# Kernel tuning notes

Hardware: AMD Instinct MI355X
Metric: run time of the kernel (lower is better)

## Reference

```python
import jax, jax.numpy as jnp
import numpy as np

WINDOW_SIZE = 11
SIGMA = 1.5


def _make_window(channel):
    # 1D gaussian, normalized, then outer product -> (C, 1, K, K) depthwise kernel
    xs = np.arange(WINDOW_SIZE) - WINDOW_SIZE // 2
    g = np.exp(-(xs ** 2) / (2.0 * SIGMA ** 2))
    g = g / g.sum()
    w2d = np.outer(g, g).astype(np.float32)
    w = np.broadcast_to(w2d[None, None], (channel, 1, WINDOW_SIZE, WINDOW_SIZE))
    return jnp.asarray(np.ascontiguousarray(w))


def _dwconv(x, window, channel):
    # depthwise valid conv, NCHW layout, groups = channel
    return jax.lax.conv_general_dilated(
        x, window,
        window_strides=(1, 1), padding='VALID',
        dimension_numbers=('NCHW', 'OIHW', 'NCHW'),
        feature_group_count=channel)


def setup_inputs() -> dict:
    key = jax.random.key(0)
    k1, k2 = jax.random.split(key)
    img1 = jax.random.uniform(k1, (32, 3, 512, 512), dtype=jnp.float32)
    img2 = jax.random.uniform(k2, (32, 3, 512, 512), dtype=jnp.float32)
    return {"img1": img1, "img2": img2}


def reference(img1, img2):
    channel = img1.shape[1]
    window = _make_window(channel).astype(img1.dtype)

    # dynamic range heuristic (val_range is None in the module's usage)
    max_val = jnp.where(jnp.max(img1) > 128, 255.0, 1.0)
    min_val = jnp.where(jnp.min(img1) < -0.5, -1.0, 0.0)
    L = max_val - min_val

    mu1 = _dwconv(img1, window, channel)
    mu2 = _dwconv(img2, window, channel)
    mu1_sq = mu1 * mu1
    mu2_sq = mu2 * mu2
    mu1_mu2 = mu1 * mu2

    sigma1_sq = _dwconv(img1 * img1, window, channel) - mu1_sq
    sigma2_sq = _dwconv(img2 * img2, window, channel) - mu2_sq
    sigma12 = _dwconv(img1 * img2, window, channel) - mu1_mu2

    C1 = (0.01 * L) ** 2
    C2 = (0.03 * L) ** 2
    ssim_map = ((2 * mu1_mu2 + C1) * (2 * sigma12 + C2)) / (
        (mu1_sq + mu2_sq + C1) * (sigma1_sq + sigma2_sq + C2))
    return 1.0 - jnp.mean(ssim_map)
```

## Files before the change

### kernel.cpp

```cpp
#include <hip/hip_runtime.h>


constexpr int W   = 512;
constexpr int H   = 512;
constexpr int NCH = 96;
constexpr int WO  = 502;
constexpr int SOUT = 118;
constexpr int NSTRIP = 5;
constexpr int ORB  = 64;
constexpr int NBAND = 8;
constexpr int NWAVE = NSTRIP * NBAND * NCH;

__device__ __constant__ const float GW[11] = {
  0.0010283885f, 0.0075987582f, 0.0360008058f, 0.1093606695f, 0.2130055279f,
  0.2660116484f,
  0.2130055279f, 0.1093606695f, 0.0360008058f, 0.0075987582f, 0.0010283885f};

__device__ __forceinline__ unsigned fkey(float f) {
  unsigned u = __float_as_uint(f);
  return (u & 0x80000000u) ? ~u : (u | 0x80000000u);
}
__device__ __forceinline__ float funkey(unsigned k) {
  unsigned u = (k & 0x80000000u) ? (k & 0x7FFFFFFFu) : ~k;
  return __uint_as_float(u);
}
__device__ __forceinline__ float bperm(int byteidx, float v) {
  return __int_as_float(__builtin_amdgcn_ds_bpermute(byteidx, __float_as_int(v)));
}

__global__ void init_ws_kernel(unsigned* ws) {
  ws[0] = 0u;
  ws[1] = 0xFFFFFFFFu;
  ((float*)ws)[2] = 0.0f;
}

__global__ __launch_bounds__(256) void minmax_kernel(
    const float4* __restrict__ x, unsigned* __restrict__ ws, int n4) {
  const int tid = threadIdx.x;
  const int gid = blockIdx.x * 256 + tid;
  const int S = gridDim.x * 256;
  float mx = -3.4e38f, mn = 3.4e38f;
  for (int i = gid; i < n4; i += 4 * S) {
    float4 v0 = x[i];
    float4 v1 = (i + S     < n4) ? x[i + S]     : v0;
    float4 v2 = (i + 2 * S < n4) ? x[i + 2 * S] : v0;
    float4 v3 = (i + 3 * S < n4) ? x[i + 3 * S] : v0;
    mx = fmaxf(mx, fmaxf(fmaxf(fmaxf(v0.x, v0.y), fmaxf(v0.z, v0.w)),
                         fmaxf(fmaxf(v1.x, v1.y), fmaxf(v1.z, v1.w))));
    mx = fmaxf(mx, fmaxf(fmaxf(fmaxf(v2.x, v2.y), fmaxf(v2.z, v2.w)),
                         fmaxf(fmaxf(v3.x, v3.y), fmaxf(v3.z, v3.w))));
    mn = fminf(mn, fminf(fminf(fminf(v0.x, v0.y), fminf(v0.z, v0.w)),
                         fminf(fminf(v1.x, v1.y), fminf(v1.z, v1.w))));
    mn = fminf(mn, fminf(fminf(fminf(v2.x, v2.y), fminf(v2.z, v2.w)),
                         fminf(fminf(v3.x, v3.y), fminf(v3.z, v3.w))));
  }
  #pragma unroll
  for (int off = 32; off; off >>= 1) {
    mx = fmaxf(mx, __shfl_down(mx, off));
    mn = fminf(mn, __shfl_down(mn, off));
  }
  __shared__ float smx[4], smn[4];
  const int lane = tid & 63, wib = tid >> 6;
  if (lane == 0) { smx[wib] = mx; smn[wib] = mn; }
  __syncthreads();
  if (tid == 0) {
    mx = fmaxf(fmaxf(smx[0], smx[1]), fmaxf(smx[2], smx[3]));
    mn = fminf(fminf(smn[0], smn[1]), fminf(smn[2], smn[3]));
    atomicMax(&ws[0], fkey(mx));
    atomicMin(&ws[1], fkey(mn));
  }
}

__global__ __launch_bounds__(256) void ssim_kernel(
    const float* __restrict__ img1, const float* __restrict__ img2,
    const unsigned* __restrict__ wsk, float* __restrict__ sum_out) {
  const int tid  = threadIdx.x;
  const int lane = tid & 63;
  const int wib  = tid >> 6;
  const int wid  = blockIdx.x * 4 + wib;

  const int strip = wid % NSTRIP;
  const int band  = (wid / NSTRIP) % NBAND;
  const int plane = wid / (NSTRIP * NBAND);

  const int O0 = strip * SOUT;
  const int r0 = band * ORB;
  const int c0 = O0 + (lane << 1);
  const bool cok = (c0 < W);

  const float* p1 = img1 + (size_t)plane * (H * W);
  const float* p2 = img2 + (size_t)plane * (H * W);

  const float maxv = funkey(wsk[0]);
  const float minv = funkey(wsk[1]);
  const float L = (maxv > 128.0f ? 255.0f : 1.0f) - (minv < -0.5f ? -1.0f : 0.0f);
  float C1 = 0.01f * L; C1 *= C1;
  float C2 = 0.03f * L; C2 *= C2;

  const int im3 = ((lane - 3) & 63) << 2;
  const int im2 = ((lane - 2) & 63) << 2;
  const int im1 = ((lane - 1) & 63) << 2;
  const int ip1 = ((lane + 1) & 63) << 2;
  const int ip2 = ((lane + 2) & 63) << 2;

  float acc[11][5][2];
  #pragma unroll
  for (int s = 0; s < 11; ++s)
    #pragma unroll
    for (int q = 0; q < 5; ++q) { acc[s][q][0] = 0.f; acc[s][q][1] = 0.f; }

  float lsum = 0.f;

  float na0 = 0.f, na1 = 0.f, nb0 = 0.f, nb1 = 0.f;
  if (cok) {
    float2 t1 = *reinterpret_cast<const float2*>(p1 + (size_t)r0 * W + c0);
    float2 t2 = *reinterpret_cast<const float2*>(p2 + (size_t)r0 * W + c0);
    na0 = t1.x; na1 = t1.y; nb0 = t2.x; nb1 = t2.y;
  }

  #pragma unroll 1
  for (int g = 0; g < 7; ++g) {
    #pragma unroll
    for (int p = 0; p < 11; ++p) {
      const float ca0 = na0, ca1 = na1, cb0 = nb0, cb1 = nb1;

      const int rn = r0 + 11 * g + p + 1;
      if ((rn < H) && cok) {
        float2 t1 = *reinterpret_cast<const float2*>(p1 + (size_t)rn * W + c0);
        float2 t2 = *reinterpret_cast<const float2*>(p2 + (size_t)rn * W + c0);
        na0 = t1.x; na1 = t1.y; nb0 = t2.x; nb1 = t2.y;
      } else {
        na0 = 0.f; na1 = 0.f; nb0 = 0.f; nb1 = 0.f;
      }

      float wa[12], wb[12];
      wa[6] = ca0; wa[7] = ca1; wb[6] = cb0; wb[7] = cb1;
      wa[0]  = bperm(im3, ca0); wa[1]  = bperm(im3, ca1);
      wa[2]  = bperm(im2, ca0); wa[3]  = bperm(im2, ca1);
      wa[4]  = bperm(im1, ca0); wa[5]  = bperm(im1, ca1);
      wa[8]  = bperm(ip1, ca0); wa[9]  = bperm(ip1, ca1);
      wa[10] = bperm(ip2, ca0); wa[11] = bperm(ip2, ca1);
      wb[0]  = bperm(im3, cb0); wb[1]  = bperm(im3, cb1);
      wb[2]  = bperm(im2, cb0); wb[3]  = bperm(im2, cb1);
      wb[4]  = bperm(im1, cb0); wb[5]  = bperm(im1, cb1);
      wb[8]  = bperm(ip1, cb0); wb[9]  = bperm(ip1, cb1);
      wb[10] = bperm(ip2, cb0); wb[11] = bperm(ip2, cb1);

      float h[5][2];
      h[0][0] = 0.f; h[0][1] = 0.f; h[1][0] = 0.f; h[1][1] = 0.f;
      #pragma unroll
      for (int k = 0; k < 11; ++k) {
        h[0][0] = fmaf(GW[k], wa[k],     h[0][0]);
        h[0][1] = fmaf(GW[k], wa[k + 1], h[0][1]);
        h[1][0] = fmaf(GW[k], wb[k],     h[1][0]);
        h[1][1] = fmaf(GW[k], wb[k + 1], h[1][1]);
      }
      {
        float sq[12];
        #pragma unroll
        for (int m = 0; m < 12; ++m) sq[m] = wa[m] * wa[m];
        h[2][0] = 0.f; h[2][1] = 0.f;
        #pragma unroll
        for (int k = 0; k < 11; ++k) {
          h[2][0] = fmaf(GW[k], sq[k],     h[2][0]);
          h[2][1] = fmaf(GW[k], sq[k + 1], h[2][1]);
        }
      }
      {
        float sq[12];
        #pragma unroll
        for (int m = 0; m < 12; ++m) sq[m] = wb[m] * wb[m];
        h[3][0] = 0.f; h[3][1] = 0.f;
        #pragma unroll
        for (int k = 0; k < 11; ++k) {
          h[3][0] = fmaf(GW[k], sq[k],     h[3][0]);
          h[3][1] = fmaf(GW[k], sq[k + 1], h[3][1]);
        }
      }
      {
        float sq[12];
        #pragma unroll
        for (int m = 0; m < 12; ++m) sq[m] = wa[m] * wb[m];
        h[4][0] = 0.f; h[4][1] = 0.f;
        #pragma unroll
        for (int k = 0; k < 11; ++k) {
          h[4][0] = fmaf(GW[k], sq[k],     h[4][0]);
          h[4][1] = fmaf(GW[k], sq[k + 1], h[4][1]);
        }
      }

      #pragma unroll
      for (int s = 0; s < 11; ++s) {
        const float wv = GW[(p - s + 11) % 11];
        #pragma unroll
        for (int q = 0; q < 5; ++q) {
          acc[s][q][0] = fmaf(wv, h[q][0], acc[s][q][0]);
          acc[s][q][1] = fmaf(wv, h[q][1], acc[s][q][1]);
        }
      }

      const int es = (p + 1) % 11;
      const int ol = 11 * g + p - 10;
      const int orow = r0 + ol;
      if (ol >= 0 && ol < ORB && orow < WO) {
        #pragma unroll
        for (int c = 0; c < 2; ++c) {
          const int ocol = c0 - 6 + c;
          const bool valid = (lane >= 3) && (lane <= 61) && (ocol < WO);
          const float mu1 = acc[es][0][c], mu2 = acc[es][1][c];
          const float m11 = mu1 * mu1, m22 = mu2 * mu2, m12 = mu1 * mu2;
          const float s11 = acc[es][2][c] - m11;
          const float s22 = acc[es][3][c] - m22;
          const float s12 = acc[es][4][c] - m12;
          const float num = (2.f * m12 + C1) * (2.f * s12 + C2);
          const float den = (m11 + m22 + C1) * (s11 + s22 + C2);
          lsum += valid ? num * __builtin_amdgcn_rcpf(den) : 0.f;
        }
      }
      #pragma unroll
      for (int q = 0; q < 5; ++q) { acc[es][q][0] = 0.f; acc[es][q][1] = 0.f; }
    }
  }

  #pragma unroll
  for (int off = 32; off; off >>= 1) lsum += __shfl_down(lsum, off);
  __shared__ float bsum[4];
  if (lane == 0) bsum[wib] = lsum;
  __syncthreads();
  if (tid == 0) atomicAdd(sum_out, bsum[0] + bsum[1] + bsum[2] + bsum[3]);
}

__global__ void finalize_kernel(const float* __restrict__ sum, float* __restrict__ out) {
  out[0] = 1.0f - sum[0] * (1.0f / 24192384.0f);
}

extern "C" void kernel_launch(void* const* d_in, const int* in_sizes, int n_in,
                              void* d_out, int out_size, void* d_ws, size_t ws_size,
                              hipStream_t stream) {
  const float* img1 = (const float*)d_in[0];
  const float* img2 = (const float*)d_in[1];
  float* out = (float*)d_out;
  unsigned* ws = (unsigned*)d_ws;

  init_ws_kernel<<<1, 1, 0, stream>>>(ws);

  int n4 = in_sizes[0] >> 2;
  minmax_kernel<<<2048, 256, 0, stream>>>((const float4*)img1, ws, n4);

  ssim_kernel<<<NWAVE / 4, 256, 0, stream>>>(img1, img2, ws, (float*)ws + 2);

  finalize_kernel<<<1, 1, 0, stream>>>((const float*)ws + 2, out);
}
```

Before: 425.1 us.

## Merge sigma1+sigma2 filter, shrink row bands, fold finalize into last block

Combines the img1^2 and img2^2 separable filters into one filter of their sum, since only sigma1+sigma2 is needed. This drops one of the five filtered quantities and its accumulators. Row bands shrink from 64 to 42 rows, giving 12 bands and more waves, at the cost of more halo rows per output. The init and finalize kernels become a memset plus a last-block completion counter, and the min is encoded as an inverted atomicMax so zero-init works; this trims launches but adds atomics and fences.

```diff
diff --git a/kernel.cpp b/kernel.cpp
--- a/kernel.cpp
+++ b/kernel.cpp
@@ -7,9 +7,11 @@
 constexpr int WO  = 502;
 constexpr int SOUT = 118;
 constexpr int NSTRIP = 5;
-constexpr int ORB  = 64;
-constexpr int NBAND = 8;
+constexpr int ORB  = 42;
+constexpr int NBAND = 12;
+constexpr int NG   = 5;
 constexpr int NWAVE = NSTRIP * NBAND * NCH;
+constexpr int NBLOCK = NWAVE / 4;
 
 __device__ __constant__ const float GW[11] = {
   0.0010283885f, 0.0075987582f, 0.0360008058f, 0.1093606695f, 0.2130055279f,
@@ -26,12 +28,6 @@
 }
 __device__ __forceinline__ float bperm(int byteidx, float v) {
   return __int_as_float(__builtin_amdgcn_ds_bpermute(byteidx, __float_as_int(v)));
-}
-
-__global__ void init_ws_kernel(unsigned* ws) {
-  ws[0] = 0u;
-  ws[1] = 0xFFFFFFFFu;
-  ((float*)ws)[2] = 0.0f;
 }
 
 __global__ __launch_bounds__(256) void minmax_kernel(
@@ -67,13 +63,13 @@
     mx = fmaxf(fmaxf(smx[0], smx[1]), fmaxf(smx[2], smx[3]));
     mn = fminf(fminf(smn[0], smn[1]), fminf(smn[2], smn[3]));
     atomicMax(&ws[0], fkey(mx));
-    atomicMin(&ws[1], fkey(mn));
+    atomicMax(&ws[1], ~fkey(mn));
   }
 }
 
 __global__ __launch_bounds__(256) void ssim_kernel(
     const float* __restrict__ img1, const float* __restrict__ img2,
-    const unsigned* __restrict__ wsk, float* __restrict__ sum_out) {
+    unsigned* __restrict__ ws, float* __restrict__ out) {
   const int tid  = threadIdx.x;
   const int lane = tid & 63;
   const int wib  = tid >> 6;
@@ -91,8 +87,8 @@
   const float* p1 = img1 + (size_t)plane * (H * W);
   const float* p2 = img2 + (size_t)plane * (H * W);
 
-  const float maxv = funkey(wsk[0]);
-  const float minv = funkey(wsk[1]);
+  const float maxv = funkey(ws[0]);
+  const float minv = funkey(~ws[1]);
   const float L = (maxv > 128.0f ? 255.0f : 1.0f) - (minv < -0.5f ? -1.0f : 0.0f);
   float C1 = 0.01f * L; C1 *= C1;
   float C2 = 0.03f * L; C2 *= C2;
@@ -103,11 +99,11 @@
   const int ip1 = ((lane + 1) & 63) << 2;
   const int ip2 = ((lane + 2) & 63) << 2;
 
-  float acc[11][5][2];
+  float acc[11][4][2];
   #pragma unroll
   for (int s = 0; s < 11; ++s)
     #pragma unroll
-    for (int q = 0; q < 5; ++q) { acc[s][q][0] = 0.f; acc[s][q][1] = 0.f; }
+    for (int q = 0; q < 4; ++q) { acc[s][q][0] = 0.f; acc[s][q][1] = 0.f; }
 
   float lsum = 0.f;
 
@@ -119,7 +115,7 @@
   }
 
   #pragma unroll 1
-  for (int g = 0; g < 7; ++g) {
+  for (int g = 0; g < NG; ++g) {
     #pragma unroll
     for (int p = 0; p < 11; ++p) {
       const float ca0 = na0, ca1 = na1, cb0 = nb0, cb1 = nb1;
@@ -146,7 +142,7 @@
       wb[8]  = bperm(ip1, cb0); wb[9]  = bperm(ip1, cb1);
       wb[10] = bperm(ip2, cb0); wb[11] = bperm(ip2, cb1);
 
-      float h[5][2];
+      float h[4][2];
       h[0][0] = 0.f; h[0][1] = 0.f; h[1][0] = 0.f; h[1][1] = 0.f;
       #pragma unroll
       for (int k = 0; k < 11; ++k) {
@@ -156,36 +152,25 @@
         h[1][1] = fmaf(GW[k], wb[k + 1], h[1][1]);
       }
       {
-        float sq[12];
-        #pragma unroll
-        for (int m = 0; m < 12; ++m) sq[m] = wa[m] * wa[m];
+        float t[12];
+        #pragma unroll
+        for (int m = 0; m < 12; ++m) t[m] = fmaf(wa[m], wa[m], wb[m] * wb[m]);
         h[2][0] = 0.f; h[2][1] = 0.f;
         #pragma unroll
         for (int k = 0; k < 11; ++k) {
-          h[2][0] = fmaf(GW[k], sq[k],     h[2][0]);
-          h[2][1] = fmaf(GW[k], sq[k + 1], h[2][1]);
+          h[2][0] = fmaf(GW[k], t[k],     h[2][0]);
+          h[2][1] = fmaf(GW[k], t[k + 1], h[2][1]);
         }
       }
       {
-        float sq[12];
-        #pragma unroll
-        for (int m = 0; m < 12; ++m) sq[m] = wb[m] * wb[m];
+        float t[12];
+        #pragma unroll
+        for (int m = 0; m < 12; ++m) t[m] = wa[m] * wb[m];
         h[3][0] = 0.f; h[3][1] = 0.f;
         #pragma unroll
         for (int k = 0; k < 11; ++k) {
-          h[3][0] = fmaf(GW[k], sq[k],     h[3][0]);
-          h[3][1] = fmaf(GW[k], sq[k + 1], h[3][1]);
-        }
-      }
-      {
-        float sq[12];
-        #pragma unroll
-        for (int m = 0; m < 12; ++m) sq[m] = wa[m] * wb[m];
-        h[4][0] = 0.f; h[4][1] = 0.f;
-        #pragma unroll
-        for (int k = 0; k < 11; ++k) {
-          h[4][0] = fmaf(GW[k], sq[k],     h[4][0]);
-          h[4][1] = fmaf(GW[k], sq[k + 1], h[4][1]);
+          h[3][0] = fmaf(GW[k], t[k],     h[3][0]);
+          h[3][1] = fmaf(GW[k], t[k + 1], h[3][1]);
         }
       }
 
@@ -193,7 +178,7 @@
       for (int s = 0; s < 11; ++s) {
         const float wv = GW[(p - s + 11) % 11];
         #pragma unroll
-        for (int q = 0; q < 5; ++q) {
+        for (int q = 0; q < 4; ++q) {
           acc[s][q][0] = fmaf(wv, h[q][0], acc[s][q][0]);
           acc[s][q][1] = fmaf(wv, h[q][1], acc[s][q][1]);
         }
@@ -209,16 +194,15 @@
           const bool valid = (lane >= 3) && (lane <= 61) && (ocol < WO);
           const float mu1 = acc[es][0][c], mu2 = acc[es][1][c];
           const float m11 = mu1 * mu1, m22 = mu2 * mu2, m12 = mu1 * mu2;
-          const float s11 = acc[es][2][c] - m11;
-          const float s22 = acc[es][3][c] - m22;
-          const float s12 = acc[es][4][c] - m12;
+          const float ssum = acc[es][2][c] - m11 - m22;
+          const float s12  = acc[es][3][c] - m12;
           const float num = (2.f * m12 + C1) * (2.f * s12 + C2);
-          const float den = (m11 + m22 + C1) * (s11 + s22 + C2);
+          const float den = (m11 + m22 + C1) * (ssum + C2);
           lsum += valid ? num * __builtin_amdgcn_rcpf(den) : 0.f;
         }
       }
       #pragma unroll
-      for (int q = 0; q < 5; ++q) { acc[es][q][0] = 0.f; acc[es][q][1] = 0.f; }
+      for (int q = 0; q < 4; ++q) { acc[es][q][0] = 0.f; acc[es][q][1] = 0.f; }
     }
   }
 
@@ -227,11 +211,17 @@
   __shared__ float bsum[4];
   if (lane == 0) bsum[wib] = lsum;
   __syncthreads();
-  if (tid == 0) atomicAdd(sum_out, bsum[0] + bsum[1] + bsum[2] + bsum[3]);
-}
-
-__global__ void finalize_kernel(const float* __restrict__ sum, float* __restrict__ out) {
-  out[0] = 1.0f - sum[0] * (1.0f / 24192384.0f);
+  if (tid == 0) {
+    const float part = bsum[0] + bsum[1] + bsum[2] + bsum[3];
+    atomicAdd((float*)&ws[2], part);
+    __threadfence();
+    const unsigned prev = atomicAdd(&ws[3], 1u);
+    if (prev == (unsigned)(NBLOCK - 1)) {
+      __threadfence();
+      const float total = atomicAdd((float*)&ws[2], 0.0f);
+      out[0] = 1.0f - total * (1.0f / 24192384.0f);
+    }
+  }
 }
 
 extern "C" void kernel_launch(void* const* d_in, const int* in_sizes, int n_in,
@@ -242,12 +232,10 @@
   float* out = (float*)d_out;
   unsigned* ws = (unsigned*)d_ws;
 
-  init_ws_kernel<<<1, 1, 0, stream>>>(ws);
+  hipMemsetAsync(ws, 0, 16, stream);
 
   int n4 = in_sizes[0] >> 2;
   minmax_kernel<<<2048, 256, 0, stream>>>((const float4*)img1, ws, n4);
 
-  ssim_kernel<<<NWAVE / 4, 256, 0, stream>>>(img1, img2, ws, (float*)ws + 2);
-
-  finalize_kernel<<<1, 1, 0, stream>>>((const float*)ws + 2, out);
-}
+  ssim_kernel<<<NBLOCK, 256, 0, stream>>>(img1, img2, ws, out);
+}
```

New measurement: 450.5 us. 6.0% more time.
